# Performance work log

Measured on AMD Instinct MI355X. Metric: run time of the kernel, lower is better.

## Reference

```python
import jax, jax.numpy as jnp
import numpy as np

INPUT_SIZE = 256
NUM_LABELS = 50
L = NUM_LABELS + 1  # internal label count incl. pad label (index L-1)
B, T = 64, 256


def setup_inputs() -> dict:
    key = jax.random.key(0)
    k = jax.random.split(key, 8)
    inp = {
        "input": jax.random.normal(k[0], (B, T, INPUT_SIZE), dtype=jnp.float32),
        "mask": jnp.ones((B, T), dtype=jnp.float32),
        "target": jax.random.randint(k[1], (B, T), 0, NUM_LABELS),
        # state_nn: Linear(input_size, L)
        "state_W": jax.random.normal(k[2], (INPUT_SIZE, L), dtype=jnp.float32) * 0.05,
        "state_b": jnp.zeros((L,), dtype=jnp.float32),
        # trans_nn: Linear(input_size, L*L) (bigram=True)
        "trans_W": jax.random.normal(k[3], (INPUT_SIZE, L * L), dtype=jnp.float32) * 0.05,
        "trans_b": jnp.zeros((L * L,), dtype=jnp.float32),
    }
    return inp


def _energy(x, mask, state_W, state_b, trans_W, trans_b):
    # out_s: [B,T,L]  (unary scores), out_t: [B,T,L,L] (bigram transitions)
    out_s = jnp.einsum("bti,il->btl", x, state_W) + state_b
    out_t = (jnp.einsum("bti,io->bto", x, trans_W) + trans_b).reshape(
        x.shape[0], x.shape[1], L, L
    )
    energy = out_t + out_s[:, :, None, :]  # [B,T,L,L]
    return energy * mask[:, :, None, None]


def reference(input, mask, target, state_W, state_b, trans_W, trans_b):
    """ChainCRF.loss: -log p(target | input) per batch element, shape [B]."""
    energy = _energy(input, mask, state_W, state_b, trans_W, trans_b)
    e_t = jnp.transpose(energy, (1, 0, 2, 3))  # [T,B,L,L]
    tgt_t = target.T                            # [T,B]
    msk_t = mask.T                              # [T,B]
    bidx = jnp.arange(input.shape[0])

    # t = 0: start from pad label (index L-1)
    partition0 = e_t[0][:, L - 1, :]                       # [B,L]
    tgt0 = e_t[0][bidx, L - 1, tgt_t[0]]                   # [B]

    def step(carry, xs):
        part, tgt_e, prev = carry
        curr, tgt, m = xs  # curr [B,L,L], tgt [B], m [B]
        part_new = jax.nn.logsumexp(curr + part[:, :, None], axis=1)
        part = part + (part_new - part) * m[:, None]
        tgt_e = tgt_e + curr[bidx, prev, tgt]
        return (part, tgt_e, tgt), None

    (part, tgt_e, _), _ = jax.lax.scan(
        step, (partition0, tgt0, tgt_t[0]), (e_t[1:], tgt_t[1:], msk_t[1:])
    )
    return jax.nn.logsumexp(part, axis=1) - tgt_e
```

## Files before the change

kernel.cpp:

```cpp
#include <hip/hip_runtime.h>
#include <hip/hip_bf16.h>

#define B_    64
#define T_    256
#define K_    256
#define L_    51
#define LL_   2601
#define RS_   64
#define NG_   3328
#define PSTP_ 3328
#define PSTQ_ 4096
#define MT_   128
#define NT_   128
#define LOG2E_ 1.4426950408889634f

typedef __bf16 bf16x8 __attribute__((ext_vector_type(8)));
typedef float  f32x4  __attribute__((ext_vector_type(4)));
typedef unsigned int u32x4 __attribute__((ext_vector_type(4)));
typedef u32x4 __attribute__((may_alias)) u32x4_a;
typedef unsigned long long ull;
typedef ull __attribute__((may_alias)) ull_a;
typedef unsigned short ushort_a __attribute__((may_alias));

static __device__ __forceinline__ bf16x8 as_bf16x8(u32x4 u) {
    return __builtin_bit_cast(bf16x8, u);
}
static __device__ __forceinline__ unsigned short bf16bits(float x) {
    return __builtin_bit_cast(unsigned short, __float2bfloat16(x));
}
static __device__ __forceinline__ ull pack4(f32x4 a) {
    return (ull)bf16bits(a[0]) | ((ull)bf16bits(a[1]) << 16) |
           ((ull)bf16bits(a[2]) << 32) | ((ull)bf16bits(a[3]) << 48);
}
static __device__ __forceinline__ void gld_lds16(const void* g, void* l) {
    __builtin_amdgcn_global_load_lds(
        (const __attribute__((address_space(1))) unsigned int*)g,
        (__attribute__((address_space(3))) unsigned int*)l, 16, 0, 0);
}

#define DPP_STEP(v, OP, CTRL)                                                   \
    {                                                                           \
        int _x = __builtin_bit_cast(int, v);                                    \
        float _o = __builtin_bit_cast(                                          \
            float, __builtin_amdgcn_update_dpp(_x, _x, CTRL, 0xF, 0xF, true));  \
        v = OP(v, _o);                                                          \
    }
static __device__ __forceinline__ float addf(float a, float b) { return a + b; }

__global__ __launch_bounds__(256) void prep_all(
    const float* __restrict__ trans_W, const float* __restrict__ trans_b,
    const float* __restrict__ state_W, const float* __restrict__ state_b,
    const float* __restrict__ x,
    __hip_bfloat16* __restrict__ Wt, float* __restrict__ bias,
    __hip_bfloat16* __restrict__ xb)
{
    __shared__ __align__(16) __hip_bfloat16 Wl[52 * 258];
    const int blk = blockIdx.x, tid = threadIdx.x;

    if (blk < 64) {
        const int i = blk;
        if (i < L_) {
            const int jp = tid & 63, kk = tid >> 6;
            if (jp < 52) {
                for (int k = kk; k < K_; k += 4) {
                    float v = 0.f;
                    if (jp < L_) v = (trans_W[(size_t)k * LL_ + i * L_ + jp] +
                                      state_W[k * L_ + jp]) * LOG2E_;
                    Wl[jp * 258 + k] = __float2bfloat16(v);
                }
            }
            __syncthreads();
            for (int idx = tid; idx < 52 * 32; idx += 256) {
                const int j = idx >> 5, c = idx & 31;
                const unsigned int* row = (const unsigned int*)&Wl[j * 258];
                u32x4 v;
                v[0] = row[c * 4 + 0]; v[1] = row[c * 4 + 1];
                v[2] = row[c * 4 + 2]; v[3] = row[c * 4 + 3];
                *(u32x4*)(Wt + (size_t)((j << 6) + i) * K_ + c * 8) = v;
            }
        } else {
            const u32x4 z = {};
            for (int idx = tid; idx < 52 * 32; idx += 256) {
                const int j = idx >> 5, c = idx & 31;
                *(u32x4*)(Wt + (size_t)((j << 6) + i) * K_ + c * 8) = z;
            }
        }
        if (tid < 52) {
            const int j = tid;
            bias[(j << 6) + i] =
                (i < L_ && j < L_) ? (trans_b[i * L_ + j] + state_b[j]) * LOG2E_
                                   : 0.f;
        }
    } else {
        const int n4 = B_ * T_ * K_ / 4;
        const float4* x4 = (const float4*)x;
        ushort4* xb4 = (ushort4*)xb;
        for (int idx = (blk - 64) * 256 + tid; idx < n4; idx += 1024 * 256) {
            float4 v = x4[idx];
            ushort4 o;
            o.x = bf16bits(v.x); o.y = bf16bits(v.y);
            o.z = bf16bits(v.z); o.w = bf16bits(v.w);
            xb4[idx] = o;
        }
    }
}

__global__ __launch_bounds__(256) void gemm_energy(
    const __hip_bfloat16* __restrict__ xb,
    const __hip_bfloat16* __restrict__ Wt,
    const float* __restrict__ bias,
    const float* __restrict__ mask,
    __hip_bfloat16* __restrict__ P,
    int t0, int Tc, int TcShift)
{
    __shared__ __align__(16) char smem[66048];
    float* msk_sh = (float*)(smem + 65536);

    const int tid  = threadIdx.x;
    const int lane = tid & 63;
    const int wv   = tid >> 6;
    const int quad = lane >> 4;
    const int l16  = lane & 15;
    const int m0 = blockIdx.y * MT_;
    const int n0 = blockIdx.x * NT_;
    const int mrow0 = (wv >> 1) * 64;
    const int ncol0 = (wv & 1) * 64;

    float bv[4];
#pragma unroll
    for (int nf = 0; nf < 4; ++nf) bv[nf] = bias[n0 + ncol0 + nf * 16 + l16];

    const char* asrc[4]; const char* bsrc[4]; char* adst[4]; char* bdst[4];
#pragma unroll
    for (int it = 0; it < 4; ++it) {
        const int s = it * 256 + tid;
        const int r = s >> 3;
        const int c = (lane & 7) ^ (r & 7);
        const int ma = m0 + r;
        const int rg = (ma >> TcShift) * T_ + t0 + (ma & (Tc - 1));
        asrc[it] = (const char*)xb + (size_t)rg * 512 + c * 16;
        bsrc[it] = (const char*)Wt + (size_t)(n0 + r) * 512 + c * 16;
        adst[it] = smem + it * 4096 + wv * 1024;
        bdst[it] = smem + 32768 + it * 4096 + wv * 1024;
    }
    auto stage = [&](int kp, int bsel) {
#pragma unroll
        for (int it = 0; it < 4; ++it) {
            gld_lds16(asrc[it] + kp * 128, adst[it] + bsel * 16384);
            gld_lds16(bsrc[it] + kp * 128, bdst[it] + bsel * 16384);
        }
    };

    stage(0, 0);

    f32x4 acc[4][4];
#pragma unroll
    for (int mf = 0; mf < 4; ++mf)
#pragma unroll
        for (int nf = 0; nf < 4; ++nf)
            acc[mf][nf] = (f32x4){bv[nf], bv[nf], bv[nf], bv[nf]};

#pragma unroll
    for (int kp = 0; kp < 4; ++kp) {
        if (kp < 3) {
            stage(kp + 1, (kp + 1) & 1);
            asm volatile("s_waitcnt vmcnt(8)" ::: "memory");
        } else {
            asm volatile("s_waitcnt vmcnt(0)" ::: "memory");
        }
        __builtin_amdgcn_s_barrier();
        const u32x4_a* Av = (const u32x4_a*)(smem + (kp & 1) * 16384);
        const u32x4_a* Bv = (const u32x4_a*)(smem + 32768 + (kp & 1) * 16384);
        __builtin_amdgcn_s_setprio(1);
#pragma unroll
        for (int kk = 0; kk < 2; ++kk) {
            bf16x8 af[4], bfr[4];
#pragma unroll
            for (int f = 0; f < 4; ++f) {
                const int ra = mrow0 + f * 16 + l16;
                af[f]  = as_bf16x8(Av[ra * 8 + ((kk * 4 + quad) ^ (ra & 7))]);
                const int rb = ncol0 + f * 16 + l16;
                bfr[f] = as_bf16x8(Bv[rb * 8 + ((kk * 4 + quad) ^ (rb & 7))]);
            }
#pragma unroll
            for (int mf = 0; mf < 4; ++mf)
#pragma unroll
                for (int nf = 0; nf < 4; ++nf)
                    acc[mf][nf] = __builtin_amdgcn_mfma_f32_16x16x32_bf16(
                        af[mf], bfr[nf], acc[mf][nf], 0, 0, 0);
        }
        __builtin_amdgcn_s_setprio(0);
        asm volatile("s_waitcnt lgkmcnt(0)" ::: "memory");
        __builtin_amdgcn_s_barrier();
    }

    if (tid < 128) {
        const int m = m0 + tid;
        msk_sh[tid] = mask[(m >> TcShift) * T_ + t0 + (m & (Tc - 1))];
    }
    __syncthreads();

    char* E = smem;
    const int jcol = (n0 + ncol0) >> 6;
    const bool jok = jcol < L_;
    const float mlane = msk_sh[mrow0 + lane];
    const bool fastw = __all(mlane == 1.f);
    const int colb0 = (ncol0 + l16) * 2;

    if (!jok) {
#pragma unroll
        for (int mf = 0; mf < 4; ++mf)
#pragma unroll
            for (int r = 0; r < 4; ++r) {
                char* erow = E + (mrow0 + mf * 16 + quad * 4 + r) * 272;
#pragma unroll
                for (int nf = 0; nf < 4; ++nf)
                    *(ushort_a*)(erow + colb0 + nf * 32) = 0;
            }
    } else if (fastw) {
        const bool ok3 = (l16 < 3);
#pragma unroll
        for (int mf = 0; mf < 4; ++mf)
#pragma unroll
            for (int r = 0; r < 4; ++r) {
                char* erow = E + (mrow0 + mf * 16 + quad * 4 + r) * 272;
#pragma unroll
                for (int nf = 0; nf < 4; ++nf) {
                    float v = __builtin_exp2f(acc[mf][nf][r]);
                    if (nf == 3) v = ok3 ? v : 0.f;
                    *(ushort_a*)(erow + colb0 + nf * 32) = bf16bits(v);
                }
            }
    } else {
#pragma unroll
        for (int mf = 0; mf < 4; ++mf)
#pragma unroll
            for (int r = 0; r < 4; ++r) {
                const int ml = mrow0 + mf * 16 + quad * 4 + r;
                const int t  = t0 + ((m0 + ml) & (Tc - 1));
                const float mval = msk_sh[ml];
                const bool idm = (mval == 0.f) && (t != 0);
                char* erow = E + ml * 272;
#pragma unroll
                for (int nf = 0; nf < 4; ++nf) {
                    const bool okn = (nf < 3) || (l16 < 3);
                    const int ii = nf * 16 + l16;
                    float v;
                    if (idm) v = (okn && ii == jcol) ? 1.f : 0.f;
                    else     v = okn ? __builtin_exp2f(acc[mf][nf][r] * mval) : 0.f;
                    *(ushort_a*)(erow + colb0 + nf * 32) = bf16bits(v);
                }
            }
    }
    __syncthreads();

#pragma unroll
    for (int it2 = 0; it2 < 8; ++it2) {
        const int idx = it2 * 256 + tid;
        const int ml = idx >> 4, c = idx & 15;
        const u32x4 v = *(const u32x4_a*)(E + ml * 272 + c * 16);
        *(u32x4*)(P + (size_t)(m0 + ml) * PSTP_ + n0 + c * 8) = v;
    }
}

__global__ __launch_bounds__(256) void prod_quad(
    const __hip_bfloat16* __restrict__ P,
    __hip_bfloat16* __restrict__ Q,
    int Tc)
{
    __shared__ u32x4 Sm[4][512];
    __shared__ __align__(16) unsigned short Tb[2][64 * 64];

    unsigned short* W2t = (unsigned short*)&Sm[0][0];
    unsigned short* W4b = (unsigned short*)&Sm[2][0];

    const int tid  = threadIdx.x;
    const int wv   = tid >> 6;
    const int lane = tid & 63;
    const int quad = lane >> 4;
    const int l16  = lane & 15;
    const int bq = blockIdx.x;
    const int Tq = Tc >> 2;
    const int b  = bq / Tq;
    const int tq = bq - b * Tq;
    const __hip_bfloat16* tile0 = P + (size_t)(b * Tc + tq * 4) * PSTP_;

    {
        const u32x4 z = {};
        for (int i2 = tid; i2 < 4 * 96; i2 += 256) {
            const int tile = i2 / 96;
            const int pos  = i2 - tile * 96;
            Sm[tile][416 + pos] = z;
        }
    }
#pragma unroll
    for (int part = 0; part < 7; ++part) {
        const int slot = part * 64 + lane;
        const int r    = slot >> 3;
        if (r < 52) {
            const int csrc = (slot & 7) ^ (r & 7);
            gld_lds16((const char*)(tile0 + (size_t)wv * PSTP_) + (r * 8 + csrc) * 16,
                      (char*)&Sm[wv][part * 64]);
        }
    }

    u32x4 idf[2];
    {
        const int e = l16 & 7;
        const unsigned int bits = (e & 1) ? 0x3F800000u : 0x3F80u;
#pragma unroll
        for (int par = 0; par < 2; ++par) {
            u32x4 v = {};
            if (quad == (l16 >> 3) + par * 2) v[e >> 1] = bits;
            idf[par] = v;
        }
    }

    auto twr = [&](unsigned short* buf, int rb, int colb, ull v) {
        *(ull_a*)((char*)buf + rb * 128 + ((colb + 16 * (rb & 7)) & 127)) = v;
    };
    auto trd = [&](const unsigned short* buf, int r, int colb) -> u32x4 {
        return *(const u32x4_a*)((char*)buf + r * 128 + ((colb + 16 * (r & 7)) & 127));
    };
    const int wcol = wv * 32 + quad * 8;

    const int ra = wv * 16 + l16;
    const f32x4 z = {};
    asm volatile("s_waitcnt vmcnt(0)" ::: "memory");
    __syncthreads();

#pragma unroll
    for (int tt = 0; tt < 2; ++tt) {
        const u32x4* S = Sm[tt * 2];
        bf16x8 a0 = as_bf16x8(S[ra * 8 + (quad ^ (ra & 7))]);
        bf16x8 a1 = as_bf16x8(S[ra * 8 + ((4 + quad) ^ (ra & 7))]);
#pragma unroll
        for (int nf = 0; nf < 4; ++nf) {
            f32x4 d = __builtin_amdgcn_mfma_f32_16x16x32_bf16(
                (nf >> 1) ? a1 : a0, as_bf16x8(idf[nf & 1]), z, 0, 0, 0);
            twr(Tb[tt], nf * 16 + l16, wcol, pack4(d));
        }
    }
    __syncthreads();

    {
        bf16x8 a2[2], a3[2];
#pragma unroll
        for (int ks = 0; ks < 2; ++ks) {
            a2[ks] = as_bf16x8(Sm[1][ra * 8 + ((ks * 4 + quad) ^ (ra & 7))]);
            a3[ks] = as_bf16x8(trd(Tb[1], ra, ks * 64 + quad * 16));
        }
        ull w2v[4], w4v[4];
#pragma unroll
        for (int nf = 0; nf < 4; ++nf) {
            const int rb = nf * 16 + l16;
            f32x4 u = z, v = z;
#pragma unroll
            for (int ks = 0; ks < 2; ++ks) {
                bf16x8 bU = as_bf16x8(trd(Tb[0], rb, ks * 64 + quad * 16));
                bf16x8 bV = as_bf16x8(Sm[3][rb * 8 + ((ks * 4 + quad) ^ (rb & 7))]);
                u = __builtin_amdgcn_mfma_f32_16x16x32_bf16(a2[ks], bU, u, 0, 0, 0);
                v = __builtin_amdgcn_mfma_f32_16x16x32_bf16(a3[ks], bV, v, 0, 0, 0);
            }
            w2v[nf] = pack4(u);
            w4v[nf] = pack4(v);
        }
        __syncthreads();
#pragma unroll
        for (int nf = 0; nf < 4; ++nf) {
            twr(W2t, nf * 16 + l16, wcol, w2v[nf]);
            twr(W4b, nf * 16 + l16, wcol, w4v[nf]);
        }
    }
    __syncthreads();

    {
        bf16x8 aw[2];
#pragma unroll
        for (int ks = 0; ks < 2; ++ks)
            aw[ks] = as_bf16x8(trd(W2t, ra, ks * 64 + quad * 16));
        ull mv[4];
#pragma unroll
        for (int nf = 0; nf < 4; ++nf) {
            const int rb = nf * 16 + l16;
            f32x4 d = z;
#pragma unroll
            for (int ks = 0; ks < 2; ++ks) {
                bf16x8 bw = as_bf16x8(trd(W4b, rb, ks * 64 + quad * 16));
                d = __builtin_amdgcn_mfma_f32_16x16x32_bf16(aw[ks], bw, d, 0, 0, 0);
            }
            mv[nf] = pack4(d);
        }
        __syncthreads();
#pragma unroll
        for (int nf = 0; nf < 4; ++nf)
            twr(Tb[0], nf * 16 + l16, wcol, mv[nf]);
    }
    __syncthreads();

    u32x4* qout = (u32x4*)(Q + (size_t)bq * PSTQ_);
#pragma unroll
    for (int c = tid; c < 512; c += 256) {
        const int row = c >> 3;
        const int pos = c & 7;
        qout[row * 8 + pos] = trd(Tb[0], row, pos * 16);
    }
}

__global__ __launch_bounds__(128, 1) void scan_q(
    const __hip_bfloat16* __restrict__ Q,
    const __hip_bfloat16* __restrict__ P,
    const int* __restrict__ target, const float* __restrict__ mask,
    float* __restrict__ p_ws, float* __restrict__ ls_ws,
    float* __restrict__ tgt_ws, float* __restrict__ out,
    int t0q, int Tq, int Tqtot)
{
    __shared__ __align__(16) unsigned short p_arr[64];
    __shared__ float tgt_sh;

    const int b    = blockIdx.x;
    const int tid  = threadIdx.x;
    const int wv   = tid >> 6;
    const int lane = tid & 63;
    const int quad = lane >> 4;
    const int l16  = lane & 15;
    const int t0 = t0q << 2, Tc = Tq << 2;

    float pv[4] = {0.f, 0.f, 0.f, 0.f};
    float logscale = 0.f;

    if (wv == 0) {
        if (t0q == 0) {
            p_arr[lane] = (lane == L_ - 1) ? (unsigned short)0x3F80 : (unsigned short)0;
        } else {
#pragma unroll
            for (int f = 0; f < 4; ++f) pv[f] = p_ws[b * 64 + f * 16 + l16];
            logscale = ls_ws[b];
            p_arr[quad * 16 + l16] = bf16bits(pv[quad]);
        }
        asm volatile("s_waitcnt lgkmcnt(0)" ::: "memory");

        int off[8];
#pragma unroll
        for (int f = 0; f < 4; ++f)
#pragma unroll
            for (int ks = 0; ks < 2; ++ks)
                off[f * 2 + ks] = (f * 16 + l16) * 8 + ks * 4 + quad;

        const u32x4* gp = (const u32x4*)Q + (size_t)b * Tq * (PSTQ_ / 8);
        const u32x4_a* pa = (const u32x4_a*)p_arr;

        u32x4 s0[8], s1[8], s2[8], s3[8];
        auto fetch = [&](u32x4 (&st)[8], int tl) {
            const u32x4* g = gp + (size_t)tl * (PSTQ_ / 8);
#pragma unroll
            for (int q = 0; q < 8; ++q) st[q] = g[off[q]];
        };
        fetch(s0, 0);
        if (1 < Tq) fetch(s1, 1);
        if (2 < Tq) fetch(s2, 2);
        if (3 < Tq) fetch(s3, 3);

        auto step = [&](u32x4 (&st)[8], int tl) {
            bf16x8 a0 = as_bf16x8(pa[quad]);
            bf16x8 a1 = as_bf16x8(pa[4 + quad]);
            const f32x4 z = {};
            f32x4 ae[4], ao[4];
#pragma unroll
            for (int f = 0; f < 4; ++f) {
                ae[f] = __builtin_amdgcn_mfma_f32_16x16x32_bf16(a0, as_bf16x8(st[f * 2 + 0]), z, 0, 0, 0);
                ao[f] = __builtin_amdgcn_mfma_f32_16x16x32_bf16(a1, as_bf16x8(st[f * 2 + 1]), z, 0, 0, 0);
            }
#pragma unroll
            for (int f = 0; f < 4; ++f) pv[f] = ae[f][0] + ao[f][0];

            if (((tl & 1) == 1) || (tl == Tq - 1)) {
                float mx = fmaxf(fmaxf(pv[0], pv[1]), fmaxf(pv[2], pv[3]));
                DPP_STEP(mx, fmaxf, 0xB1);
                DPP_STEP(mx, fmaxf, 0x4E);
                DPP_STEP(mx, fmaxf, 0x124);
                DPP_STEP(mx, fmaxf, 0x128);
                const float inv = 1.f / mx;
                logscale += __logf(mx);
#pragma unroll
                for (int f = 0; f < 4; ++f) pv[f] *= inv;
            }
            p_arr[quad * 16 + l16] = bf16bits(pv[quad]);
            asm volatile("s_waitcnt lgkmcnt(0)" ::: "memory");
        };

        for (int tl = 0; tl < Tq; tl += 4) {
            step(s0, tl);
            if (tl + 4 < Tq) fetch(s0, tl + 4);
            if (tl + 1 < Tq) { step(s1, tl + 1); if (tl + 5 < Tq) fetch(s1, tl + 5); }
            if (tl + 2 < Tq) { step(s2, tl + 2); if (tl + 6 < Tq) fetch(s2, tl + 6); }
            if (tl + 3 < Tq) { step(s3, tl + 3); if (tl + 7 < Tq) fetch(s3, tl + 7); }
        }
    } else {
        float s = 0.f;
        for (int tl = lane; tl < Tc; tl += 64) {
            const int t = t0 + tl;
            const int j = target[b * T_ + t];
            const int i = (t == 0) ? (L_ - 1) : target[b * T_ + t - 1];
            const float m = (t == 0) ? 1.f : mask[b * T_ + t];
            if (m != 0.f) {
                const float pval =
                    __bfloat162float(P[(size_t)(b * Tc + tl) * PSTP_ + j * RS_ + i]);
                s += __logf(pval);
            }
        }
#pragma unroll
        for (int d = 1; d < 64; d <<= 1) s += __shfl_xor(s, d);
        if (lane == 0) {
            const float tot = (t0 == 0) ? s : tgt_ws[b] + s;
            tgt_ws[b] = tot;
            tgt_sh = tot;
        }
    }
    __syncthreads();

    if (wv == 0) {
        if (t0q + Tq == Tqtot) {
            float s = pv[0] + pv[1] + pv[2] + pv[3];
            DPP_STEP(s, addf, 0xB1);
            DPP_STEP(s, addf, 0x4E);
            DPP_STEP(s, addf, 0x124);
            DPP_STEP(s, addf, 0x128);
            if (lane == 0) out[b] = logscale + __logf(s) - tgt_sh;
        } else {
            if (quad == 0) {
#pragma unroll
                for (int f = 0; f < 4; ++f) p_ws[b * 64 + f * 16 + l16] = pv[f];
            }
            if (lane == 0) ls_ws[b] = logscale;
        }
    }
}

extern "C" void kernel_launch(void* const* d_in, const int* in_sizes, int n_in,
                              void* d_out, int out_size, void* d_ws, size_t ws_size,
                              hipStream_t stream)
{
    (void)in_sizes; (void)n_in; (void)out_size;
    const float* x       = (const float*)d_in[0];
    const float* mask    = (const float*)d_in[1];
    const int*   target  = (const int*)d_in[2];
    const float* state_W = (const float*)d_in[3];
    const float* state_b = (const float*)d_in[4];
    const float* trans_W = (const float*)d_in[5];
    const float* trans_b = (const float*)d_in[6];
    float* out = (float*)d_out;

    char* ws = (char*)d_ws;
    size_t off = 0;
    auto alloc = [&](size_t bytes) -> void* {
        void* p = ws + off;
        off = (off + bytes + 255) & ~(size_t)255;
        return p;
    };

    __hip_bfloat16* Wt   = (__hip_bfloat16*)alloc((size_t)NG_ * K_ * 2);
    float*          bias = (float*)alloc((size_t)NG_ * 4);
    __hip_bfloat16* xb   = (__hip_bfloat16*)alloc((size_t)B_ * T_ * K_ * 2);
    float*          p_ws = (float*)alloc((size_t)B_ * 64 * 4);
    float*          ls   = (float*)alloc((size_t)B_ * 4);
    float*          tgte = (float*)alloc((size_t)B_ * 4);
    const size_t fixed = off;

    int Tc = 256;
    while (Tc > 4 && fixed + (size_t)Tc * B_ * PSTP_ * 2
                   + (size_t)(Tc / 4) * B_ * PSTQ_ * 2 + 1024 > ws_size)
        Tc >>= 1;
    __hip_bfloat16* P = (__hip_bfloat16*)alloc((size_t)Tc * B_ * PSTP_ * 2);
    __hip_bfloat16* Q = (__hip_bfloat16*)alloc((size_t)(Tc / 4) * B_ * PSTQ_ * 2);
    int TcShift = 0;
    while ((1 << TcShift) < Tc) ++TcShift;

    prep_all<<<dim3(1088), 256, 0, stream>>>(
        trans_W, trans_b, state_W, state_b, x, Wt, bias, xb);

    for (int t0 = 0; t0 < T_; t0 += Tc) {
        gemm_energy<<<dim3(NG_ / NT_, (B_ * Tc) / MT_), 256, 0, stream>>>(
            xb, Wt, bias, mask, P, t0, Tc, TcShift);
        prod_quad<<<dim3(B_ * (Tc / 4)), 256, 0, stream>>>(P, Q, Tc);
        scan_q<<<dim3(B_), 128, 0, stream>>>(Q, P, target, mask, p_ws, ls, tgte, out,
                                             t0 / 4, Tc / 4, T_ / 4);
    }
}
```

Before: 197.9 us.

## Halve GEMM shared memory via smaller K stages, swizzled block order, rotated epilogue

Cuts the gemm_energy shared-memory footprint from about 66KB to 32KB by staging K in 32-element chunks over 8 iterations instead of 64-element chunks over 4. This should allow more blocks per CU. It also remaps the block index to a 1D grid grouped by 8 M-tiles for better L2 reuse of the weight tiles, and reads the mask per lane with a shuffle instead of through shared memory. The epilogue tile now uses a 256-byte row stride with a per-row rotation in place of padding, so it fits in the smaller buffer. The cost is more barriers and pipeline steps per tile, and the epilogue reads become two 8-byte loads instead of one 16-byte load.

```diff
diff --git a/kernel.cpp b/kernel.cpp
--- a/kernel.cpp
+++ b/kernel.cpp
@@ -111,43 +111,59 @@
     const float* __restrict__ bias,
     const float* __restrict__ mask,
     __hip_bfloat16* __restrict__ P,
-    int t0, int Tc, int TcShift)
+    int t0, int Tc, int TcShift, int swz)
 {
-    __shared__ __align__(16) char smem[66048];
-    float* msk_sh = (float*)(smem + 65536);
+    __shared__ __align__(16) char smem[32768];
 
     const int tid  = threadIdx.x;
     const int lane = tid & 63;
     const int wv   = tid >> 6;
     const int quad = lane >> 4;
     const int l16  = lane & 15;
-    const int m0 = blockIdx.y * MT_;
-    const int n0 = blockIdx.x * NT_;
+
+    int xt, yt;
+    if (swz) {
+        const int r8 = blockIdx.x & 7;
+        const int h  = blockIdx.x >> 3;
+        const int qd = h / 26;
+        xt = h - qd * 26;
+        yt = r8 + 8 * qd;
+    } else {
+        const int qd = blockIdx.x / 26;
+        xt = blockIdx.x - qd * 26;
+        yt = qd;
+    }
+    const int m0 = yt * MT_;
+    const int n0 = xt * NT_;
     const int mrow0 = (wv >> 1) * 64;
     const int ncol0 = (wv & 1) * 64;
 
     float bv[4];
 #pragma unroll
     for (int nf = 0; nf < 4; ++nf) bv[nf] = bias[n0 + ncol0 + nf * 16 + l16];
-
-    const char* asrc[4]; const char* bsrc[4]; char* adst[4]; char* bdst[4];
-#pragma unroll
-    for (int it = 0; it < 4; ++it) {
+    const int mrowg = m0 + mrow0 + lane;
+    const float mlane =
+        mask[(mrowg >> TcShift) * T_ + t0 + (mrowg & (Tc - 1))];
+
+    const char* asrc[2]; const char* bsrc[2]; char* adst[2]; char* bdst[2];
+#pragma unroll
+    for (int it = 0; it < 2; ++it) {
         const int s = it * 256 + tid;
-        const int r = s >> 3;
-        const int c = (lane & 7) ^ (r & 7);
+        const int r = s >> 2;
+        const int cs = (lane & 3) ^ (r & 3);
         const int ma = m0 + r;
         const int rg = (ma >> TcShift) * T_ + t0 + (ma & (Tc - 1));
-        asrc[it] = (const char*)xb + (size_t)rg * 512 + c * 16;
-        bsrc[it] = (const char*)Wt + (size_t)(n0 + r) * 512 + c * 16;
+        asrc[it] = (const char*)xb + (size_t)rg * 512 + cs * 16;
+        bsrc[it] = (const char*)Wt + (size_t)(n0 + r) * 512 + cs * 16;
         adst[it] = smem + it * 4096 + wv * 1024;
-        bdst[it] = smem + 32768 + it * 4096 + wv * 1024;
+        bdst[it] = smem + 16384 + it * 4096 + wv * 1024;
     }
     auto stage = [&](int kp, int bsel) {
-#pragma unroll
-        for (int it = 0; it < 4; ++it) {
-            gld_lds16(asrc[it] + kp * 128, adst[it] + bsel * 16384);
-            gld_lds16(bsrc[it] + kp * 128, bdst[it] + bsel * 16384);
+        const int ko = kp * 64;
+#pragma unroll
+        for (int it = 0; it < 2; ++it) {
+            gld_lds16(asrc[it] + ko, adst[it] + bsel * 8192);
+            gld_lds16(bsrc[it] + ko, bdst[it] + bsel * 8192);
         }
     };
 
@@ -161,49 +177,40 @@
             acc[mf][nf] = (f32x4){bv[nf], bv[nf], bv[nf], bv[nf]};
 
 #pragma unroll
-    for (int kp = 0; kp < 4; ++kp) {
-        if (kp < 3) {
+    for (int kp = 0; kp < 8; ++kp) {
+        if (kp < 7) {
             stage(kp + 1, (kp + 1) & 1);
-            asm volatile("s_waitcnt vmcnt(8)" ::: "memory");
+            asm volatile("s_waitcnt vmcnt(4)" ::: "memory");
         } else {
             asm volatile("s_waitcnt vmcnt(0)" ::: "memory");
         }
         __builtin_amdgcn_s_barrier();
-        const u32x4_a* Av = (const u32x4_a*)(smem + (kp & 1) * 16384);
-        const u32x4_a* Bv = (const u32x4_a*)(smem + 32768 + (kp & 1) * 16384);
+        const u32x4_a* Av = (const u32x4_a*)(smem + (kp & 1) * 8192);
+        const u32x4_a* Bv = (const u32x4_a*)(smem + 16384 + (kp & 1) * 8192);
         __builtin_amdgcn_s_setprio(1);
-#pragma unroll
-        for (int kk = 0; kk < 2; ++kk) {
-            bf16x8 af[4], bfr[4];
-#pragma unroll
-            for (int f = 0; f < 4; ++f) {
-                const int ra = mrow0 + f * 16 + l16;
-                af[f]  = as_bf16x8(Av[ra * 8 + ((kk * 4 + quad) ^ (ra & 7))]);
-                const int rb = ncol0 + f * 16 + l16;
-                bfr[f] = as_bf16x8(Bv[rb * 8 + ((kk * 4 + quad) ^ (rb & 7))]);
-            }
-#pragma unroll
-            for (int mf = 0; mf < 4; ++mf)
-#pragma unroll
-                for (int nf = 0; nf < 4; ++nf)
-                    acc[mf][nf] = __builtin_amdgcn_mfma_f32_16x16x32_bf16(
-                        af[mf], bfr[nf], acc[mf][nf], 0, 0, 0);
-        }
+        bf16x8 af[4], bfr[4];
+#pragma unroll
+        for (int f = 0; f < 4; ++f) {
+            const int ra = mrow0 + f * 16 + l16;
+            af[f]  = as_bf16x8(Av[ra * 4 + (quad ^ (ra & 3))]);
+            const int rb = ncol0 + f * 16 + l16;
+            bfr[f] = as_bf16x8(Bv[rb * 4 + (quad ^ (rb & 3))]);
+        }
+#pragma unroll
+        for (int mf = 0; mf < 4; ++mf)
+#pragma unroll
+            for (int nf = 0; nf < 4; ++nf)
+                acc[mf][nf] = __builtin_amdgcn_mfma_f32_16x16x32_bf16(
+                    af[mf], bfr[nf], acc[mf][nf], 0, 0, 0);
         __builtin_amdgcn_s_setprio(0);
         asm volatile("s_waitcnt lgkmcnt(0)" ::: "memory");
-        __builtin_amdgcn_s_barrier();
-    }
-
-    if (tid < 128) {
-        const int m = m0 + tid;
-        msk_sh[tid] = mask[(m >> TcShift) * T_ + t0 + (m & (Tc - 1))];
+        if (kp < 7) __builtin_amdgcn_s_barrier();
     }
     __syncthreads();
 
     char* E = smem;
     const int jcol = (n0 + ncol0) >> 6;
     const bool jok = jcol < L_;
-    const float mlane = msk_sh[mrow0 + lane];
     const bool fastw = __all(mlane == 1.f);
     const int colb0 = (ncol0 + l16) * 2;
 
@@ -212,10 +219,12 @@
         for (int mf = 0; mf < 4; ++mf)
 #pragma unroll
             for (int r = 0; r < 4; ++r) {
-                char* erow = E + (mrow0 + mf * 16 + quad * 4 + r) * 272;
+                const int ml = mrow0 + mf * 16 + quad * 4 + r;
+                char* erow = E + ml * 256;
+                const int rot = (ml * 8) & 255;
 #pragma unroll
                 for (int nf = 0; nf < 4; ++nf)
-                    *(ushort_a*)(erow + colb0 + nf * 32) = 0;
+                    *(ushort_a*)(erow + ((colb0 + nf * 32 + rot) & 255)) = 0;
             }
     } else if (fastw) {
         const bool ok3 = (l16 < 3);
@@ -223,12 +232,15 @@
         for (int mf = 0; mf < 4; ++mf)
 #pragma unroll
             for (int r = 0; r < 4; ++r) {
-                char* erow = E + (mrow0 + mf * 16 + quad * 4 + r) * 272;
+                const int ml = mrow0 + mf * 16 + quad * 4 + r;
+                char* erow = E + ml * 256;
+                const int rot = (ml * 8) & 255;
 #pragma unroll
                 for (int nf = 0; nf < 4; ++nf) {
                     float v = __builtin_exp2f(acc[mf][nf][r]);
                     if (nf == 3) v = ok3 ? v : 0.f;
-                    *(ushort_a*)(erow + colb0 + nf * 32) = bf16bits(v);
+                    *(ushort_a*)(erow + ((colb0 + nf * 32 + rot) & 255)) =
+                        bf16bits(v);
                 }
             }
     } else {
@@ -238,9 +250,10 @@
             for (int r = 0; r < 4; ++r) {
                 const int ml = mrow0 + mf * 16 + quad * 4 + r;
                 const int t  = t0 + ((m0 + ml) & (Tc - 1));
-                const float mval = msk_sh[ml];
+                const float mval = __shfl(mlane, ml - mrow0);
                 const bool idm = (mval == 0.f) && (t != 0);
-                char* erow = E + ml * 272;
+                char* erow = E + ml * 256;
+                const int rot = (ml * 8) & 255;
 #pragma unroll
                 for (int nf = 0; nf < 4; ++nf) {
                     const bool okn = (nf < 3) || (l16 < 3);
@@ -248,7 +261,8 @@
                     float v;
                     if (idm) v = (okn && ii == jcol) ? 1.f : 0.f;
                     else     v = okn ? __builtin_exp2f(acc[mf][nf][r] * mval) : 0.f;
-                    *(ushort_a*)(erow + colb0 + nf * 32) = bf16bits(v);
+                    *(ushort_a*)(erow + ((colb0 + nf * 32 + rot) & 255)) =
+                        bf16bits(v);
                 }
             }
     }
@@ -258,7 +272,13 @@
     for (int it2 = 0; it2 < 8; ++it2) {
         const int idx = it2 * 256 + tid;
         const int ml = idx >> 4, c = idx & 15;
-        const u32x4 v = *(const u32x4_a*)(E + ml * 272 + c * 16);
+        const char* erow = E + ml * 256;
+        const int rot = (ml * 8) & 255;
+        const ull lo = *(const ull_a*)(erow + ((c * 16 + rot) & 255));
+        const ull hi = *(const ull_a*)(erow + ((c * 16 + 8 + rot) & 255));
+        u32x4 v;
+        v[0] = (unsigned int)lo; v[1] = (unsigned int)(lo >> 32);
+        v[2] = (unsigned int)hi; v[3] = (unsigned int)(hi >> 32);
         *(u32x4*)(P + (size_t)(m0 + ml) * PSTP_ + n0 + c * 8) = v;
     }
 }
@@ -580,8 +600,10 @@
         trans_W, trans_b, state_W, state_b, x, Wt, bias, xb);
 
     for (int t0 = 0; t0 < T_; t0 += Tc) {
-        gemm_energy<<<dim3(NG_ / NT_, (B_ * Tc) / MT_), 256, 0, stream>>>(
-            xb, Wt, bias, mask, P, t0, Tc, TcShift);
+        const int mtiles = (B_ * Tc) / MT_;
+        const int swz = (mtiles % 8 == 0) ? 1 : 0;
+        gemm_energy<<<dim3((NG_ / NT_) * mtiles), 256, 0, stream>>>(
+            xb, Wt, bias, mask, P, t0, Tc, TcShift, swz);
         prod_quad<<<dim3(B_ * (Tc / 4)), 256, 0, stream>>>(P, Q, Tc);
         scan_q<<<dim3(B_), 128, 0, stream>>>(Q, P, target, mask, p_ws, ls, tgte, out,
                                              t0 / 4, Tc / 4, T_ / 4);
```

New measurement: 194.6 us. Within noise of the previous version (-1.7%).
